# Kernel optimization log

Hardware: AMD Instinct MI355X
Metric: run time of the kernel (lower is better)

The kernel has to match this reference:

```python
import jax, jax.numpy as jnp
import numpy as np

# FitzHugh-Nagumo / Model_FN constants (from __init__)
A_ = 0.7; B_ = 0.8; EPI = 0.2; TAU = 0.1; I_ = 1.0; K_ = 1.0; W_ = 1.0
STRENGTH = 1.0; UMAX = 10.0; D_SM = 0.1; EPS_REG = 1e-3
DIM = 1024; N = 4096


def smooth_relu(x, d=D_SM):
    r = jnp.maximum(x, 0.0)
    sq = (2.0 * d * r ** 3 - r ** 4) / (2.0 * d ** 3)
    return jnp.where(r < d, sq, x - d / 2.0)


def temp_L(t, P):
    # vectorized version of Model_FN.temp_L: sum_i eig_i * v_i^T v_i, i=1..dim-1
    dim = P.shape[0]
    i = jnp.arange(1, dim)
    s = 2.0 * K_ * jnp.sin(W_ * t)                      # [1]
    thresh = int(dim + 1) / 2 - 1                       # float threshold, as in source
    eig = jnp.where(i <= thresh, 1.0 + s, 1.0 - s)      # [dim-1]
    V = P[1:]                                           # [dim-1, dim]
    return V.T @ (eig[:, None] * V)                     # [dim, dim]


def control_net(x, W1, b1, W2, b2, W3, b3):
    # ControlNet.forward: u = MLP(x); bound(u * x)
    h1 = jnp.tanh(x @ W1.T + b1)
    h2 = jnp.tanh(h1 @ W2.T + b2)
    u = h2 @ W3.T + b3
    ux = u * x
    ux = jnp.where(ux < UMAX, ux, 0.0)
    return jnp.where(-UMAX < ux, ux, 0.0)


def icnn_fn(x, ws, bs, us):
    # ICNN.icnn_fn: x [N, d_in] -> z [1, N]
    xt = x.T                                            # [d_in, N]
    z = smooth_relu(ws[0] @ xt + bs[0])
    for i in range(len(us)):
        z = smooth_relu(ws[i + 1] @ xt + bs[i + 1] + jax.nn.softplus(us[i]) @ z)
    return z


def setup_inputs() -> dict:
    key = jax.random.key(0)
    ks = jax.random.split(key, 20)
    d_in = 2 * DIM
    inp = {
        'state': jax.random.normal(ks[0], (N, d_in), jnp.float32),
        't': jax.random.uniform(ks[1], (1,), jnp.float32) * 10.0,
        'P': jax.random.normal(ks[2], (DIM, DIM), jnp.float32) / np.sqrt(DIM),
        # ControlNet weights (SpectralNorm wrapper undefined in source -> plain Linear)
        'W1': jax.random.normal(ks[3], (512, d_in), jnp.float32) / np.sqrt(d_in),
        'b1': jax.random.normal(ks[4], (512,), jnp.float32) * 0.01,
        'W2': jax.random.normal(ks[5], (512, 512), jnp.float32) / np.sqrt(512),
        'b2': jax.random.normal(ks[6], (512,), jnp.float32) * 0.01,
        'W3': jax.random.normal(ks[7], (d_in, 512), jnp.float32) / np.sqrt(512),
        'b3': jax.random.normal(ks[8], (d_in,), jnp.float32) * 0.01,
        # ICNN parameters, layer_sizes=[64, 64, 1]
        'icW0': jax.random.normal(ks[9], (64, d_in), jnp.float32) / np.sqrt(d_in),
        'icb0': jax.random.normal(ks[10], (64, 1), jnp.float32) * 0.01,
        'icW1': jax.random.normal(ks[11], (64, d_in), jnp.float32) / np.sqrt(d_in),
        'icb1': jax.random.normal(ks[12], (64, 1), jnp.float32) * 0.01,
        'icW2': jax.random.normal(ks[13], (1, d_in), jnp.float32) / np.sqrt(d_in),
        'icb2': jax.random.normal(ks[14], (1, 1), jnp.float32) * 0.01,
        'icU0': jax.random.normal(ks[15], (64, 64), jnp.float32) / np.sqrt(64),
        'icU1': jax.random.normal(ks[16], (1, 64), jnp.float32) / np.sqrt(64),
    }
    return inp


def reference(state, t, P, W1, b1, W2, b2, W3, b3,
              icW0, icb0, icW1, icb1, icW2, icb2, icU0, icU1):
    dim = state.shape[1] // 2
    u, v = state[:, :dim], state[:, dim:]

    # FN drift with time-varying Laplacian coupling (Model_FN.FN)
    Lm = temp_L(t, P)                                   # [dim, dim]
    Hu = jax.nn.sigmoid(u / TAU)                        # H(u)
    du = u - u ** 3 / 3.0 - v + I_ + STRENGTH * (Hu @ Lm.T)
    dv = EPI * (u + A_ - B_ * v)
    dx = jnp.concatenate([du, dv], axis=1)              # [N, 2*dim]

    # ControlNet on synchronization deviations (Model_FN.FN_g state transform)
    st = jnp.concatenate([u - u[:, :1], v - v[:, :1]], axis=1)
    ctrl = control_net(st, W1, b1, W2, b2, W3, b3)
    dx_total = dx + ctrl

    # ICNN Lyapunov value (ICNN.forward)
    ws, bs, us = [icW0, icW1, icW2], [icb0, icb1, icb2], [icU0, icU1]
    z = icnn_fn(state, ws, bs, us)                      # [1, N]
    z0 = icnn_fn(jnp.zeros_like(state), ws, bs, us)     # [1, N]
    regular = EPS_REG * jnp.sum(state ** 2, axis=1, keepdims=True)
    V = smooth_relu(z - z0).T + regular                 # [N, 1]

    return jnp.concatenate([dx_total, V], axis=1)       # [N, 2*dim + 1]
```

## Files before the change

kernel.cpp:

```cpp
#include <hip/hip_runtime.h>
#include <hip/hip_fp8.h>
#include <cstdint>
#include <cstddef>

using short8 = __attribute__((ext_vector_type(8))) short;
using f32x4  = __attribute__((ext_vector_type(4))) float;
using bfraw  = unsigned short;

__device__ __forceinline__ bfraw f2b(float f){
  unsigned int u = __builtin_bit_cast(unsigned int, f);
  u += 0x7FFFu + ((u >> 16) & 1u);
  return (bfraw)(u >> 16);
}
__device__ __forceinline__ float b2f(bfraw h){
  unsigned int u = ((unsigned int)h) << 16;
  return __builtin_bit_cast(float, u);
}
__device__ __forceinline__ unsigned char f2f8(float f){
  __hip_fp8_e4m3 t(f);
  return (unsigned char)t.__x;
}
__device__ __forceinline__ float srelu(float x){
  float r = fmaxf(x, 0.0f);
  if (r < 0.1f){ float r2 = r * r; return (0.2f * r2 * r - r2 * r2) * 500.0f; }
  return x - 0.05f;
}
__device__ __forceinline__ float softplusf(float x){
  return (x > 15.0f) ? x : log1pf(expf(x));
}
__device__ __forceinline__ void gload16(const void* g, void* s){
  __builtin_amdgcn_global_load_lds((const __attribute__((address_space(1))) void*)g,
                                   (__attribute__((address_space(3))) void*)s, 16, 0, 0);
}
template<int N> __device__ __forceinline__ void wait_vm(){
  if constexpr (N == 0)      asm volatile("s_waitcnt vmcnt(0)" ::: "memory");
  else if constexpr (N == 2) asm volatile("s_waitcnt vmcnt(2)" ::: "memory");
  else if constexpr (N == 3) asm volatile("s_waitcnt vmcnt(3)" ::: "memory");
  else                       asm volatile("s_waitcnt vmcnt(4)" ::: "memory");
}
__device__ __forceinline__ void block_barrier(){
  __builtin_amdgcn_s_barrier();
  asm volatile("" ::: "memory");
}

constexpr size_t OFF_STATEB = 0;
constexpr size_t OFF_STATE8 = 16777216;
constexpr size_t OFF_HUB    = 25165824;
constexpr size_t OFF_PT     = 29360128;
constexpr size_t OFF_PTEIG  = 31457280;
constexpr size_t OFF_LM8    = 33554432;
constexpr size_t OFF_W1F8   = 34603008;
constexpr size_t OFF_ICWB   = 35651584;
constexpr size_t OFF_W28    = 36175872;
constexpr size_t OFF_W38    = 36438016;
constexpr size_t OFF_H18    = 37486592;
constexpr size_t OFF_H28    = 39583744;
constexpr size_t OFF_Z1F    = 41680896;
constexpr size_t OFF_Z2PRE  = 42729472;
constexpr size_t OFF_SPU0   = 43778048;
constexpr size_t OFF_SPU1   = 43794432;
constexpr size_t OFF_Z0     = 43794688;
constexpr size_t OFF_SU1    = 43794944;
constexpr size_t OFF_SV1    = 43796992;
constexpr size_t OFF_U0     = 43799040;
constexpr size_t OFF_V0     = 43815424;

__global__ __launch_bounds__(256) void prep_all(const float* __restrict__ W1,
    const float* __restrict__ icW0, const float* __restrict__ icW1,
    const float* __restrict__ W2, const float* __restrict__ W3,
    const float* __restrict__ P, const float* __restrict__ tptr,
    const float* __restrict__ icU0, const float* __restrict__ icU1,
    const float* __restrict__ icb0, const float* __restrict__ icb1, const float* __restrict__ icb2,
    const float* __restrict__ state,
    unsigned char* __restrict__ w1f8, bfraw* __restrict__ icwb,
    unsigned char* __restrict__ w28, unsigned char* __restrict__ w3f8,
    bfraw* __restrict__ PT, bfraw* __restrict__ PTeig,
    float* __restrict__ su1, float* __restrict__ sv1,
    float* __restrict__ spU0, float* __restrict__ spU1, float* __restrict__ z0out,
    bfraw* __restrict__ stateb, unsigned char* __restrict__ state8, unsigned char* __restrict__ hub8,
    float* __restrict__ u0a, float* __restrict__ v0a){
  __shared__ float smem[4288];
  const int b = blockIdx.x;
  const int t = threadIdx.x;
  if (b < 2560){
    const int i4 = (b * 256 + t) * 4;
    if (i4 >= 1048576 && i4 < 1310720){
      const float* src = (i4 < 1179648) ? icW0 : icW1;
      const int off = (i4 < 1179648) ? (i4 - 1048576) : (i4 - 1179648);
      const int dsto = i4 - 1048576;
      float4 v = *reinterpret_cast<const float4*>(src + off);
      ushort4 o;
      o.x = f2b(v.x); o.y = f2b(v.y); o.z = f2b(v.z); o.w = f2b(v.w);
      *reinterpret_cast<ushort4*>(icwb + dsto) = o;
    } else {
      const float* src; unsigned char* dst; int off;
      if (i4 < 1048576)      { src = W1; dst = w1f8; off = i4; }
      else if (i4 < 1572864) { src = W2; dst = w28;  off = i4 - 1310720; }
      else                   { src = W3; dst = w3f8; off = i4 - 1572864; }
      float4 v = *reinterpret_cast<const float4*>(src + off);
      uchar4 o;
      o.x = f2f8(v.x); o.y = f2f8(v.y); o.z = f2f8(v.z); o.w = f2f8(v.w);
      *reinterpret_cast<uchar4*>(dst + off) = o;
    }
  } else if (b < 3584){
    float (*tile)[33] = (float(*)[33])smem;
    const int idx = b - 2560;
    const int bi = idx >> 5, bj = idx & 31;
    const int tx = t & 31, ty = t >> 5;
    #pragma unroll
    for (int r = 0; r < 4; ++r){
      const int k = bj * 32 + ty + r * 8;
      const int i = bi * 32 + tx;
      tile[ty + r * 8][tx] = P[(size_t)k * 1024 + i];
    }
    __syncthreads();
    const float s = 2.0f * sinf(tptr[0]);
    #pragma unroll
    for (int r = 0; r < 4; ++r){
      const int i = bi * 32 + ty + r * 8;
      const int k = bj * 32 + tx;
      const float p = tile[tx][ty + r * 8];
      const float e = (k == 0) ? 0.0f : ((k <= 511) ? (1.0f + s) : (1.0f - s));
      PT[(size_t)i * 1024 + k] = f2b(p);
      PTeig[(size_t)i * 1024 + k] = f2b(e * p);
    }
  } else if (b < 4096){
    const int n = b - 3584;
    float a = 0.0f, bb = 0.0f;
    for (int j = t; j < 1024; j += 256) a += W1[(size_t)n * 2048 + j];
    for (int j = t; j < 1024; j += 256) bb += W1[(size_t)n * 2048 + 1024 + j];
    #pragma unroll
    for (int o = 32; o > 0; o >>= 1){ a += __shfl_down(a, o, 64); bb += __shfl_down(bb, o, 64); }
    if ((t & 63) == 0){ smem[t >> 6] = a; smem[4 + (t >> 6)] = bb; }
    __syncthreads();
    if (t == 0){
      su1[n] = smem[0] + smem[1] + smem[2] + smem[3];
      sv1[n] = smem[4] + smem[5] + smem[6] + smem[7];
    }
  } else if (b == 4096){
    float* sp  = smem;
    float* sp1 = smem + 4096;
    float* a0  = smem + 4160;
    float* a1  = smem + 4224;
    #pragma unroll
    for (int i = 0; i < 16; ++i){
      const int idx = i * 256 + t;
      const float v = softplusf(icU0[idx]);
      sp[idx] = v;
      spU0[idx] = v;
    }
    if (t < 64){
      const float v1 = softplusf(icU1[t]);
      sp1[t] = v1;
      spU1[t] = v1;
      a0[t] = srelu(icb0[t]);
    }
    __syncthreads();
    {
      const int n = t >> 2, q = t & 3;
      float sAcc = 0.0f;
      #pragma unroll
      for (int j = 0; j < 16; ++j) sAcc += sp[n * 64 + q * 16 + j] * a0[q * 16 + j];
      sAcc += __shfl_down(sAcc, 2, 64);
      sAcc += __shfl_down(sAcc, 1, 64);
      if (q == 0) a1[n] = srelu(sAcc + icb1[n]);
    }
    __syncthreads();
    if (t < 64){
      float v = sp1[t] * a1[t];
      #pragma unroll
      for (int o = 32; o > 0; o >>= 1) v += __shfl_down(v, o, 64);
      if (t == 0) z0out[0] = srelu(v + icb2[0]);
    }
  } else {
    const int row = b - 4097;
    const float* srow = state + (size_t)row * 2048;
    float4 u4 = *reinterpret_cast<const float4*>(srow + t * 4);
    float4 v4 = *reinterpret_cast<const float4*>(srow + 1024 + t * 4);
    float us[4] = {u4.x, u4.y, u4.z, u4.w};
    float vs[4] = {v4.x, v4.y, v4.z, v4.w};
    uchar4 h8, s8u, s8v;
    unsigned char* hp = reinterpret_cast<unsigned char*>(&h8);
    unsigned char* su = reinterpret_cast<unsigned char*>(&s8u);
    unsigned char* sv = reinterpret_cast<unsigned char*>(&s8v);
    #pragma unroll
    for (int i = 0; i < 4; ++i){
      const int j = t * 4 + i;
      const float u = us[i], v = vs[i];
      stateb[(size_t)row * 2048 + j] = f2b(u);
      stateb[(size_t)row * 2048 + 1024 + j] = f2b(v);
      su[i] = f2f8(u);
      sv[i] = f2f8(v);
      hp[i] = f2f8(1.0f / (1.0f + expf(-10.0f * u)));
    }
    *reinterpret_cast<uchar4*>(state8 + (size_t)row * 2048 + t * 4) = s8u;
    *reinterpret_cast<uchar4*>(state8 + (size_t)row * 2048 + 1024 + t * 4) = s8v;
    *reinterpret_cast<uchar4*>(hub8 + (size_t)row * 1024 + t * 4) = h8;
    if (t == 0){ u0a[row] = srow[0]; v0a[row] = srow[1024]; }
  }
}

__global__ __launch_bounds__(512)
void gemm_midh1(const bfraw* __restrict__ pteig, const bfraw* __restrict__ pt,
                unsigned char* __restrict__ lm8,
                const bfraw* __restrict__ stateb, const bfraw* __restrict__ icwb,
                const float* __restrict__ icb0, const float* __restrict__ icb1,
                float* __restrict__ z1f, float* __restrict__ z2pre,
                const unsigned char* __restrict__ state8, const unsigned char* __restrict__ w1f8,
                const float* __restrict__ b1, unsigned char* __restrict__ h18,
                const float* __restrict__ u0a, const float* __restrict__ v0a,
                const float* __restrict__ su1, const float* __restrict__ sv1)
{
  __shared__ char ldsRaw[73728];
  const int blk = blockIdx.x;
  const int tid = threadIdx.x;
  const int w  = tid >> 6;
  const int l  = tid & 63;
  const int lr = l & 15;
  const int q  = l >> 4;

  if (blk < 384){
    bfraw* lA = (bfraw*)ldsRaw;
    bfraw* lB = (bfraw*)(ldsRaw + 24576);
    const bool isLm = (blk < 256);
    const bfraw* A; const bfraw* B; int K, bm, bn;
    if (isLm){ A = pteig; B = pt; K = 1024; bm = blk >> 4; bn = blk & 15; }
    else     { const int i = blk - 256; A = stateb; B = icwb; K = 2048; bm = i >> 1; bn = i & 1; }
    const int wr = w >> 2;
    const int wc = w & 3;
    f32x4 acc[2] = {};
    const int nt = K >> 6;
    auto stage = [&](int buf, int k0){
      const int r = tid >> 3;
      const int kc = (tid & 7) ^ (r & 7);
      gload16(A + (size_t)(bm * 64 + r) * K + k0 + kc * 8, &lA[(size_t)buf * 4096 + (size_t)(w * 64) * 8]);
      gload16(B + (size_t)(bn * 64 + r) * K + k0 + kc * 8, &lB[(size_t)buf * 4096 + (size_t)(w * 64) * 8]);
    };
    stage(0, 0);
    stage(1, 64);
    for (int t = 0; t < nt; ++t){
      const int cur = t % 3;
      if (t == nt - 1) wait_vm<0>(); else wait_vm<2>();
      block_barrier();
      short8 aF[2][2], bF[2];
      #pragma unroll
      for (int kh = 0; kh < 2; ++kh){
        const int kch = (kh * 4 + q) ^ (lr & 7);
        #pragma unroll
        for (int m = 0; m < 2; ++m){
          const int R = wr * 32 + m * 16 + lr;
          aF[kh][m] = *reinterpret_cast<const short8*>(&lA[(size_t)cur * 4096 + (size_t)R * 64 + kch * 8]);
        }
        const int R = wc * 16 + lr;
        bF[kh] = *reinterpret_cast<const short8*>(&lB[(size_t)cur * 4096 + (size_t)R * 64 + kch * 8]);
      }
      if (t + 2 < nt) stage((t + 2) % 3, (t + 2) * 64);
      #pragma unroll
      for (int kh = 0; kh < 2; ++kh)
        #pragma unroll
        for (int m = 0; m < 2; ++m)
          acc[m] = __builtin_amdgcn_mfma_f32_16x16x32_bf16(aF[kh][m], bF[kh], acc[m], 0, 0, 0);
    }
    #pragma unroll
    for (int m = 0; m < 2; ++m){
      #pragma unroll
      for (int r = 0; r < 4; ++r){
        const int row = bm * 64 + (w >> 2) * 32 + m * 16 + q * 4 + r;
        const int c64 = (w & 3) * 16 + lr;
        const float v = acc[m][r];
        if (isLm){
          lm8[(size_t)row * 1024 + bn * 64 + c64] = f2f8(v);
        } else if (bn == 0){
          z1f[(size_t)row * 64 + c64] = srelu(v + icb0[c64]);
        } else {
          z2pre[(size_t)row * 64 + c64] = v + icb1[c64];
        }
      }
    }
  } else {
    unsigned char* lA = (unsigned char*)ldsRaw;
    unsigned char* lB = (unsigned char*)(ldsRaw + 24576);
    const int i = blk - 384;
    const int bm = i >> 2;
    const int bn = i & 3;
    const int wr = w >> 2;
    const int wc = w & 3;
    constexpr int K = 2048;
    f32x4 acc[2][2] = {};
    const int nt = K >> 7;
    auto stage = [&](int buf, int k0){
      {
        const int c = tid;
        const int r = c >> 3;
        const int kc = (c & 7) ^ (r & 7);
        gload16(state8 + (size_t)(bm * 64 + r) * K + k0 + kc * 16, &lA[(size_t)buf * 8192 + (size_t)(w * 64) * 16]);
      }
      #pragma unroll
      for (int j = 0; j < 2; ++j){
        const int c = j * 512 + tid;
        const int r = c >> 3;
        const int kc = (c & 7) ^ (r & 7);
        gload16(w1f8 + (size_t)(bn * 128 + r) * K + k0 + kc * 16, &lB[(size_t)buf * 16384 + (size_t)(j * 512 + w * 64) * 16]);
      }
    };
    stage(0, 0);
    stage(1, 128);
    for (int t = 0; t < nt; ++t){
      const int cur = t % 3;
      if (t == nt - 1) wait_vm<0>(); else wait_vm<3>();
      block_barrier();
      long long aF[4][2], bF[4][2];
      #pragma unroll
      for (int kh = 0; kh < 4; ++kh){
        const int ko = kh * 32 + q * 8;
        const int ch = (ko >> 4) ^ (lr & 7);
        const int bo = ko & 15;
        #pragma unroll
        for (int m = 0; m < 2; ++m){
          const int R = wr * 32 + m * 16 + lr;
          aF[kh][m] = *reinterpret_cast<const long long*>(&lA[(size_t)cur * 8192 + (size_t)R * 128 + ch * 16 + bo]);
        }
        #pragma unroll
        for (int n = 0; n < 2; ++n){
          const int R = wc * 32 + n * 16 + lr;
          bF[kh][n] = *reinterpret_cast<const long long*>(&lB[(size_t)cur * 16384 + (size_t)R * 128 + ch * 16 + bo]);
        }
      }
      if (t + 2 < nt) stage((t + 2) % 3, (t + 2) * 128);
      #pragma unroll
      for (int kh = 0; kh < 4; ++kh)
        #pragma unroll
        for (int m = 0; m < 2; ++m)
          #pragma unroll
          for (int n = 0; n < 2; ++n)
            acc[m][n] = __builtin_amdgcn_mfma_f32_16x16x32_fp8_fp8(aF[kh][m], bF[kh][n], acc[m][n], 0, 0, 0);
    }
    #pragma unroll
    for (int m = 0; m < 2; ++m){
      #pragma unroll
      for (int n = 0; n < 2; ++n){
        #pragma unroll
        for (int r = 0; r < 4; ++r){
          const int row = bm * 64 + wr * 32 + m * 16 + q * 4 + r;
          const int col = bn * 128 + wc * 32 + n * 16 + lr;
          const float h = acc[m][n][r] - u0a[row] * su1[col] - v0a[row] * sv1[col] + b1[col];
          h18[(size_t)row * 512 + col] = f2f8(tanhf(h));
        }
      }
    }
  }
}

__global__ __launch_bounds__(512)
void gemm_h2(const unsigned char* __restrict__ A, const unsigned char* __restrict__ B,
             const float* __restrict__ bias, unsigned char* __restrict__ outf8)
{
  constexpr int N = 512, K = 512;
  __shared__ unsigned char lA[3][64 * 128];
  __shared__ unsigned char lB[3][128 * 128];
  const int tid = threadIdx.x;
  const int w  = tid >> 6;
  const int l  = tid & 63;
  const int wr = w >> 2;
  const int wc = w & 3;
  const int bm = blockIdx.x;
  const int bn = blockIdx.y;
  const int lr = l & 15;
  const int q  = l >> 4;
  f32x4 acc[2][2] = {};
  const int nt = K >> 7;
  auto stage = [&](int buf, int k0){
    {
      const int c = tid;
      const int r = c >> 3;
      const int kc = (c & 7) ^ (r & 7);
      gload16(A + (size_t)(bm * 64 + r) * K + k0 + kc * 16, &lA[buf][(size_t)(w * 64) * 16]);
    }
    #pragma unroll
    for (int j = 0; j < 2; ++j){
      const int c = j * 512 + tid;
      const int r = c >> 3;
      const int kc = (c & 7) ^ (r & 7);
      gload16(B + (size_t)(bn * 128 + r) * K + k0 + kc * 16, &lB[buf][(size_t)(j * 512 + w * 64) * 16]);
    }
  };
  stage(0, 0);
  stage(1, 128);
  for (int t = 0; t < nt; ++t){
    const int cur = t % 3;
    if (t == nt - 1) wait_vm<0>(); else wait_vm<3>();
    block_barrier();
    long long aF[4][2], bF[4][2];
    #pragma unroll
    for (int kh = 0; kh < 4; ++kh){
      const int ko = kh * 32 + q * 8;
      const int ch = (ko >> 4) ^ (lr & 7);
      const int bo = ko & 15;
      #pragma unroll
      for (int m = 0; m < 2; ++m){
        const int R = wr * 32 + m * 16 + lr;
        aF[kh][m] = *reinterpret_cast<const long long*>(&lA[cur][(size_t)R * 128 + ch * 16 + bo]);
      }
      #pragma unroll
      for (int n = 0; n < 2; ++n){
        const int R = wc * 32 + n * 16 + lr;
        bF[kh][n] = *reinterpret_cast<const long long*>(&lB[cur][(size_t)R * 128 + ch * 16 + bo]);
      }
    }
    if (t + 2 < nt) stage((t + 2) % 3, (t + 2) * 128);
    #pragma unroll
    for (int kh = 0; kh < 4; ++kh)
      #pragma unroll
      for (int m = 0; m < 2; ++m)
        #pragma unroll
        for (int n = 0; n < 2; ++n)
          acc[m][n] = __builtin_amdgcn_mfma_f32_16x16x32_fp8_fp8(aF[kh][m], bF[kh][n], acc[m][n], 0, 0, 0);
  }
  #pragma unroll
  for (int m = 0; m < 2; ++m){
    #pragma unroll
    for (int n = 0; n < 2; ++n){
      #pragma unroll
      for (int r = 0; r < 4; ++r){
        const int row = bm * 64 + wr * 32 + m * 16 + q * 4 + r;
        const int col = bn * 128 + wc * 32 + n * 16 + lr;
        outf8[(size_t)row * N + col] = f2f8(tanhf(acc[m][n][r] + bias[col]));
      }
    }
  }
}

__global__ __launch_bounds__(512, 4)
void gemm_outv2(const unsigned char* __restrict__ hub8, const unsigned char* __restrict__ lm8,
                const unsigned char* __restrict__ h2b8, const unsigned char* __restrict__ w3f8,
                const bfraw* __restrict__ stateb, const float* __restrict__ b3,
                const float* __restrict__ u0a, const float* __restrict__ v0a,
                const float* __restrict__ icW2, const float* __restrict__ z1f,
                const float* __restrict__ z2pre, const float* __restrict__ spU0,
                const float* __restrict__ spU1, const float* __restrict__ z0p,
                const float* __restrict__ icb2,
                float* __restrict__ out)
{
  __shared__ char ldsRaw[32768 + 512];
  const int blk = blockIdx.x;
  const int tid = threadIdx.x;

  if (blk >= 512){
    float* z1s = (float*)ldsRaw;
    float* s1  = (float*)(ldsRaw + 256);
    float* s2  = (float*)(ldsRaw + 288);
    const int row = blk - 512;
    if (tid < 64) z1s[tid] = z1f[(size_t)row * 64 + tid];
    ushort4 xv = reinterpret_cast<const ushort4*>(stateb + (size_t)row * 2048)[tid];
    float4 wv = reinterpret_cast<const float4*>(icW2)[tid];
    bfraw xr[4] = {xv.x, xv.y, xv.z, xv.w};
    float wr4[4] = {wv.x, wv.y, wv.z, wv.w};
    float d = 0.0f, ss = 0.0f;
    #pragma unroll
    for (int e = 0; e < 4; ++e){
      const float x = b2f(xr[e]);
      d  = fmaf(wr4[e], x, d);
      ss = fmaf(x, x, ss);
    }
    #pragma unroll
    for (int o = 32; o > 0; o >>= 1){ d += __shfl_down(d, o, 64); ss += __shfl_down(ss, o, 64); }
    if ((tid & 63) == 0){ s1[tid >> 6] = d; s2[tid >> 6] = ss; }
    __syncthreads();
    if (tid < 64){
      float acc2 = z2pre[(size_t)row * 64 + tid];
      #pragma unroll 8
      for (int j = 0; j < 64; ++j) acc2 += spU0[tid * 64 + j] * z1s[j];
      float dd = spU1[tid] * srelu(acc2);
      #pragma unroll
      for (int o = 32; o > 0; o >>= 1) dd += __shfl_down(dd, o, 64);
      if (tid == 0){
        float D = dd, S = 0.0f;
        #pragma unroll
        for (int k = 0; k < 8; ++k){ D += s1[k]; S += s2[k]; }
        const float z3 = srelu(D + icb2[0]);
        out[(size_t)row * 2049 + 2048] = srelu(z3 - z0p[0]) + 0.001f * S;
      }
    }
    return;
  }

  unsigned char* lA   = (unsigned char*)ldsRaw;
  unsigned char* lBlo = (unsigned char*)(ldsRaw + 16384);
  unsigned char* lBhi = (unsigned char*)(ldsRaw + 24576);
  const int w  = tid >> 6;
  const int l  = tid & 63;
  const int wr = w >> 2;
  const int wc = w & 3;
  const int bm = blk & 31;
  const int bn = blk >> 5;
  const int lr = l & 15;
  const int q  = l >> 4;

  const unsigned char* Au  = h2b8 + (size_t)(bm * 128) * 512;
  const unsigned char* Bwl = w3f8 + (size_t)(bn * 64) * 512;
  const unsigned char* Bwh = w3f8 + (size_t)(1024 + bn * 64) * 512;
  const unsigned char* Ah  = hub8 + (size_t)(bm * 128) * 1024;
  const unsigned char* Bl  = lm8  + (size_t)(bn * 64) * 1024;

  f32x4 acc2[4] = {};
  f32x4 acc3[4] = {};

  for (int t = 0; t < 4; ++t){
    const int k0 = t * 128;
    #pragma unroll
    for (int j = 0; j < 2; ++j){
      const int c = j * 512 + tid;
      const int r = c >> 3;
      const int kc = (c & 7) ^ (r & 7);
      gload16(Au + (size_t)r * 512 + k0 + kc * 16, &lA[(size_t)(j * 512 + w * 64) * 16]);
    }
    {
      const int r = tid >> 3;
      const int kc = (tid & 7) ^ (r & 7);
      gload16(Bwl + (size_t)r * 512 + k0 + kc * 16, &lBlo[(size_t)(w * 64) * 16]);
      gload16(Bwh + (size_t)r * 512 + k0 + kc * 16, &lBhi[(size_t)(w * 64) * 16]);
    }
    __syncthreads();
    #pragma unroll
    for (int kh = 0; kh < 4; ++kh){
      const int ko = kh * 32 + q * 8;
      const int ch = (ko >> 4) ^ (lr & 7);
      const int bo = ko & 15;
      long long aF[4], bL, bH;
      #pragma unroll
      for (int m = 0; m < 4; ++m){
        const int R = wr * 64 + m * 16 + lr;
        aF[m] = *reinterpret_cast<const long long*>(&lA[(size_t)R * 128 + ch * 16 + bo]);
      }
      const int Rb = wc * 16 + lr;
      bL = *reinterpret_cast<const long long*>(&lBlo[(size_t)Rb * 128 + ch * 16 + bo]);
      bH = *reinterpret_cast<const long long*>(&lBhi[(size_t)Rb * 128 + ch * 16 + bo]);
      #pragma unroll
      for (int m = 0; m < 4; ++m){
        acc2[m] = __builtin_amdgcn_mfma_f32_16x16x32_fp8_fp8(aF[m], bL, acc2[m], 0, 0, 0);
        acc3[m] = __builtin_amdgcn_mfma_f32_16x16x32_fp8_fp8(aF[m], bH, acc3[m], 0, 0, 0);
      }
    }
    __syncthreads();
  }

  #pragma unroll
  for (int m = 0; m < 4; ++m){
    #pragma unroll
    for (int r = 0; r < 4; ++r){
      const int row = bm * 128 + wr * 64 + m * 16 + q * 4 + r;
      const int c   = bn * 64 + wc * 16 + lr;
      const float un = acc3[m][r] + b3[1024 + c];
      const float u  = b2f(stateb[(size_t)row * 2048 + c]);
      const float vv = b2f(stateb[(size_t)row * 2048 + 1024 + c]);
      const float x  = vv - v0a[row];
      const float ux = un * x;
      const float cl = (ux < 10.0f && -10.0f < ux) ? ux : 0.0f;
      out[(size_t)row * 2049 + 1024 + c] = 0.2f * (u + 0.7f - 0.8f * vv) + cl;
    }
  }

  f32x4 acc1[4] = {};
  for (int t = 0; t < 8; ++t){
    const int k0 = t * 128;
    #pragma unroll
    for (int j = 0; j < 2; ++j){
      const int c = j * 512 + tid;
      const int r = c >> 3;
      const int kc = (c & 7) ^ (r & 7);
      gload16(Ah + (size_t)r * 1024 + k0 + kc * 16, &lA[(size_t)(j * 512 + w * 64) * 16]);
    }
    {
      const int r = tid >> 3;
      const int kc = (tid & 7) ^ (r & 7);
      gload16(Bl + (size_t)r * 1024 + k0 + kc * 16, &lBlo[(size_t)(w * 64) * 16]);
    }
    __syncthreads();
    #pragma unroll
    for (int kh = 0; kh < 4; ++kh){
      const int ko = kh * 32 + q * 8;
      const int ch = (ko >> 4) ^ (lr & 7);
      const int bo = ko & 15;
      long long aF[4], bL;
      #pragma unroll
      for (int m = 0; m < 4; ++m){
        const int R = wr * 64 + m * 16 + lr;
        aF[m] = *reinterpret_cast<const long long*>(&lA[(size_t)R * 128 + ch * 16 + bo]);
      }
      const int Rb = wc * 16 + lr;
      bL = *reinterpret_cast<const long long*>(&lBlo[(size_t)Rb * 128 + ch * 16 + bo]);
      #pragma unroll
      for (int m = 0; m < 4; ++m){
        acc1[m] = __builtin_amdgcn_mfma_f32_16x16x32_fp8_fp8(aF[m], bL, acc1[m], 0, 0, 0);
      }
    }
    __syncthreads();
  }

  #pragma unroll
  for (int m = 0; m < 4; ++m){
    #pragma unroll
    for (int r = 0; r < 4; ++r){
      const int row = bm * 128 + wr * 64 + m * 16 + q * 4 + r;
      const int c   = bn * 64 + wc * 16 + lr;
      const float un = acc2[m][r] + b3[c];
      const float u  = b2f(stateb[(size_t)row * 2048 + c]);
      const float vv = b2f(stateb[(size_t)row * 2048 + 1024 + c]);
      const float x  = u - u0a[row];
      const float ux = un * x;
      const float cl = (ux < 10.0f && -10.0f < ux) ? ux : 0.0f;
      out[(size_t)row * 2049 + c] = acc1[m][r] + u - u * u * u * (1.0f / 3.0f) - vv + 1.0f + cl;
    }
  }
}

extern "C" void kernel_launch(void* const* d_in, const int* in_sizes, int n_in,
                              void* d_out, int out_size, void* d_ws, size_t ws_size,
                              hipStream_t stream){
  (void)in_sizes; (void)n_in; (void)out_size; (void)ws_size;
  const float* state = (const float*)d_in[0];
  const float* tp    = (const float*)d_in[1];
  const float* P     = (const float*)d_in[2];
  const float* W1    = (const float*)d_in[3];
  const float* b1    = (const float*)d_in[4];
  const float* W2    = (const float*)d_in[5];
  const float* b2    = (const float*)d_in[6];
  const float* W3    = (const float*)d_in[7];
  const float* b3    = (const float*)d_in[8];
  const float* icW0  = (const float*)d_in[9];
  const float* icb0  = (const float*)d_in[10];
  const float* icW1  = (const float*)d_in[11];
  const float* icb1  = (const float*)d_in[12];
  const float* icW2  = (const float*)d_in[13];
  const float* icb2  = (const float*)d_in[14];
  const float* icU0  = (const float*)d_in[15];
  const float* icU1  = (const float*)d_in[16];
  float* out = (float*)d_out;
  char* ws = (char*)d_ws;

  bfraw* stateb = (bfraw*)(ws + OFF_STATEB);
  unsigned char* state8 = (unsigned char*)(ws + OFF_STATE8);
  unsigned char* hub8   = (unsigned char*)(ws + OFF_HUB);
  bfraw* pt     = (bfraw*)(ws + OFF_PT);
  bfraw* pteig  = (bfraw*)(ws + OFF_PTEIG);
  unsigned char* lm8  = (unsigned char*)(ws + OFF_LM8);
  unsigned char* w1f8 = (unsigned char*)(ws + OFF_W1F8);
  bfraw* icwb   = (bfraw*)(ws + OFF_ICWB);
  unsigned char* w28  = (unsigned char*)(ws + OFF_W28);
  unsigned char* w3f8 = (unsigned char*)(ws + OFF_W38);
  unsigned char* h18  = (unsigned char*)(ws + OFF_H18);
  unsigned char* h28  = (unsigned char*)(ws + OFF_H28);
  float* z1f    = (float*)(ws + OFF_Z1F);
  float* z2pre  = (float*)(ws + OFF_Z2PRE);
  float* spU0   = (float*)(ws + OFF_SPU0);
  float* spU1   = (float*)(ws + OFF_SPU1);
  float* z0     = (float*)(ws + OFF_Z0);
  float* su1    = (float*)(ws + OFF_SU1);
  float* sv1    = (float*)(ws + OFF_SV1);
  float* u0a    = (float*)(ws + OFF_U0);
  float* v0a    = (float*)(ws + OFF_V0);

  prep_all<<<dim3(8193), 256, 0, stream>>>(W1, icW0, icW1, W2, W3, P, tp,
      icU0, icU1, icb0, icb1, icb2, state,
      w1f8, icwb, w28, w3f8, pt, pteig, su1, sv1, spU0, spU1, z0,
      stateb, state8, hub8, u0a, v0a);

  gemm_midh1<<<dim3(640), 512, 0, stream>>>(pteig, pt, lm8, stateb, icwb, icb0, icb1,
      z1f, z2pre, state8, w1f8, b1, h18, u0a, v0a, su1, sv1);
  gemm_h2<<<dim3(64, 4), 512, 0, stream>>>(h18, w28, b2, h28);
  gemm_outv2<<<dim3(4608), 512, 0, stream>>>(hub8, lm8, h28, w3f8, stateb, b3, u0a, v0a,
      icW2, z1f, z2pre, spU0, spU1, z0, icb2, out);
}
```

Measured before the change: 95.37 us.

## Double-buffer LDS tiles in gemm_outv2 to overlap global loads with MFMA

Doubles the LDS footprint of the output GEMM kernel so the next K-tile's global-to-LDS loads are issued while the current tile is consumed. Partial vmcnt waits and explicit barriers replace the full __syncthreads after each load. The second GEMM loop is also moved ahead of the first epilogue, so both GEMMs run back to back. The extra LDS (about 66KB per block) may cut blocks per CU below the launch-bounds target of 4, and acc1 now stays live alongside acc2/acc3, which adds register pressure.

```diff
diff --git a/kernel.cpp b/kernel.cpp
--- a/kernel.cpp
+++ b/kernel.cpp
@@ -441,7 +441,7 @@
                 const float* __restrict__ icb2,
                 float* __restrict__ out)
 {
-  __shared__ char ldsRaw[32768 + 512];
+  __shared__ char ldsRaw[66048];
   const int blk = blockIdx.x;
   const int tid = threadIdx.x;
 
@@ -484,9 +484,9 @@
     return;
   }
 
-  unsigned char* lA   = (unsigned char*)ldsRaw;
-  unsigned char* lBlo = (unsigned char*)(ldsRaw + 16384);
-  unsigned char* lBhi = (unsigned char*)(ldsRaw + 24576);
+  unsigned char* PA   = (unsigned char*)ldsRaw;
+  unsigned char* PBlo = (unsigned char*)(ldsRaw + 32768);
+  unsigned char* PBhi = (unsigned char*)(ldsRaw + 49152);
   const int w  = tid >> 6;
   const int l  = tid & 63;
   const int wr = w >> 2;
@@ -505,22 +505,25 @@
   f32x4 acc2[4] = {};
   f32x4 acc3[4] = {};
 
-  for (int t = 0; t < 4; ++t){
+  auto stage1 = [&](int buf, int t){
     const int k0 = t * 128;
     #pragma unroll
     for (int j = 0; j < 2; ++j){
       const int c = j * 512 + tid;
       const int r = c >> 3;
       const int kc = (c & 7) ^ (r & 7);
-      gload16(Au + (size_t)r * 512 + k0 + kc * 16, &lA[(size_t)(j * 512 + w * 64) * 16]);
-    }
-    {
-      const int r = tid >> 3;
-      const int kc = (tid & 7) ^ (r & 7);
-      gload16(Bwl + (size_t)r * 512 + k0 + kc * 16, &lBlo[(size_t)(w * 64) * 16]);
-      gload16(Bwh + (size_t)r * 512 + k0 + kc * 16, &lBhi[(size_t)(w * 64) * 16]);
-    }
-    __syncthreads();
+      gload16(Au + (size_t)r * 512 + k0 + kc * 16, &PA[(size_t)buf * 16384 + (size_t)(j * 512 + w * 64) * 16]);
+    }
+    const int r = tid >> 3;
+    const int kc = (tid & 7) ^ (r & 7);
+    gload16(Bwl + (size_t)r * 512 + k0 + kc * 16, &PBlo[(size_t)buf * 8192 + (size_t)(w * 64) * 16]);
+    gload16(Bwh + (size_t)r * 512 + k0 + kc * 16, &PBhi[(size_t)buf * 8192 + (size_t)(w * 64) * 16]);
+  };
+  stage1(0, 0);
+  for (int t = 0; t < 4; ++t){
+    const int cur = t & 1;
+    if (t + 1 < 4){ stage1(cur ^ 1, t + 1); wait_vm<4>(); } else wait_vm<0>();
+    block_barrier();
     #pragma unroll
     for (int kh = 0; kh < 4; ++kh){
       const int ko = kh * 32 + q * 8;
@@ -530,18 +533,58 @@
       #pragma unroll
       for (int m = 0; m < 4; ++m){
         const int R = wr * 64 + m * 16 + lr;
-        aF[m] = *reinterpret_cast<const long long*>(&lA[(size_t)R * 128 + ch * 16 + bo]);
+        aF[m] = *reinterpret_cast<const long long*>(&PA[(size_t)cur * 16384 + (size_t)R * 128 + ch * 16 + bo]);
       }
       const int Rb = wc * 16 + lr;
-      bL = *reinterpret_cast<const long long*>(&lBlo[(size_t)Rb * 128 + ch * 16 + bo]);
-      bH = *reinterpret_cast<const long long*>(&lBhi[(size_t)Rb * 128 + ch * 16 + bo]);
+      bL = *reinterpret_cast<const long long*>(&PBlo[(size_t)cur * 8192 + (size_t)Rb * 128 + ch * 16 + bo]);
+      bH = *reinterpret_cast<const long long*>(&PBhi[(size_t)cur * 8192 + (size_t)Rb * 128 + ch * 16 + bo]);
       #pragma unroll
       for (int m = 0; m < 4; ++m){
         acc2[m] = __builtin_amdgcn_mfma_f32_16x16x32_fp8_fp8(aF[m], bL, acc2[m], 0, 0, 0);
         acc3[m] = __builtin_amdgcn_mfma_f32_16x16x32_fp8_fp8(aF[m], bH, acc3[m], 0, 0, 0);
       }
     }
-    __syncthreads();
+    block_barrier();
+  }
+
+  f32x4 acc1[4] = {};
+  auto stage2 = [&](int buf, int t){
+    const int k0 = t * 128;
+    #pragma unroll
+    for (int j = 0; j < 2; ++j){
+      const int c = j * 512 + tid;
+      const int r = c >> 3;
+      const int kc = (c & 7) ^ (r & 7);
+      gload16(Ah + (size_t)r * 1024 + k0 + kc * 16, &PA[(size_t)buf * 16384 + (size_t)(j * 512 + w * 64) * 16]);
+    }
+    const int r = tid >> 3;
+    const int kc = (tid & 7) ^ (r & 7);
+    gload16(Bl + (size_t)r * 1024 + k0 + kc * 16, &PBlo[(size_t)buf * 8192 + (size_t)(w * 64) * 16]);
+  };
+  stage2(0, 0);
+  for (int t = 0; t < 8; ++t){
+    const int cur = t & 1;
+    if (t + 1 < 8){ stage2(cur ^ 1, t + 1); wait_vm<3>(); } else wait_vm<0>();
+    block_barrier();
+    #pragma unroll
+    for (int kh = 0; kh < 4; ++kh){
+      const int ko = kh * 32 + q * 8;
+      const int ch = (ko >> 4) ^ (lr & 7);
+      const int bo = ko & 15;
+      long long aF[4], bL;
+      #pragma unroll
+      for (int m = 0; m < 4; ++m){
+        const int R = wr * 64 + m * 16 + lr;
+        aF[m] = *reinterpret_cast<const long long*>(&PA[(size_t)cur * 16384 + (size_t)R * 128 + ch * 16 + bo]);
+      }
+      const int Rb = wc * 16 + lr;
+      bL = *reinterpret_cast<const long long*>(&PBlo[(size_t)cur * 8192 + (size_t)Rb * 128 + ch * 16 + bo]);
+      #pragma unroll
+      for (int m = 0; m < 4; ++m){
+        acc1[m] = __builtin_amdgcn_mfma_f32_16x16x32_fp8_fp8(aF[m], bL, acc1[m], 0, 0, 0);
+      }
+    }
+    block_barrier();
   }
 
   #pragma unroll
@@ -559,44 +602,6 @@
       out[(size_t)row * 2049 + 1024 + c] = 0.2f * (u + 0.7f - 0.8f * vv) + cl;
     }
   }
-
-  f32x4 acc1[4] = {};
-  for (int t = 0; t < 8; ++t){
-    const int k0 = t * 128;
-    #pragma unroll
-    for (int j = 0; j < 2; ++j){
-      const int c = j * 512 + tid;
-      const int r = c >> 3;
-      const int kc = (c & 7) ^ (r & 7);
-      gload16(Ah + (size_t)r * 1024 + k0 + kc * 16, &lA[(size_t)(j * 512 + w * 64) * 16]);
-    }
-    {
-      const int r = tid >> 3;
-      const int kc = (tid & 7) ^ (r & 7);
-      gload16(Bl + (size_t)r * 1024 + k0 + kc * 16, &lBlo[(size_t)(w * 64) * 16]);
-    }
-    __syncthreads();
-    #pragma unroll
-    for (int kh = 0; kh < 4; ++kh){
-      const int ko = kh * 32 + q * 8;
-      const int ch = (ko >> 4) ^ (lr & 7);
-      const int bo = ko & 15;
-      long long aF[4], bL;
-      #pragma unroll
-      for (int m = 0; m < 4; ++m){
-        const int R = wr * 64 + m * 16 + lr;
-        aF[m] = *reinterpret_cast<const long long*>(&lA[(size_t)R * 128 + ch * 16 + bo]);
-      }
-      const int Rb = wc * 16 + lr;
-      bL = *reinterpret_cast<const long long*>(&lBlo[(size_t)Rb * 128 + ch * 16 + bo]);
-      #pragma unroll
-      for (int m = 0; m < 4; ++m){
-        acc1[m] = __builtin_amdgcn_mfma_f32_16x16x32_fp8_fp8(aF[m], bL, acc1[m], 0, 0, 0);
-      }
-    }
-    __syncthreads();
-  }
-
   #pragma unroll
   for (int m = 0; m < 4; ++m){
     #pragma unroll
```

Measured after the change: 100.7 us. 1.06x slower.
